# Kernel optimization log

Measured on AMD Instinct MI355X. Metric: run time of the kernel, lower is better.

## Reference

```python
import jax, jax.numpy as jnp
import numpy as np

K_SIZE = 7  # kernel_size (odd)


def setup_inputs() -> dict:
    key = jax.random.key(0)
    k0, k1, k2, k3 = jax.random.split(key, 4)
    B, C, H, W = 4, 128, 192, 192
    O, K = 128, K_SIZE
    x = jax.random.normal(k0, (B, C, H, W), dtype=jnp.float32)
    offsets = jax.random.normal(k1, (B, K, H, W), dtype=jnp.float32) * 0.5
    tumor_center = jax.random.uniform(k2, (B, 2), dtype=jnp.float32) * H  # (h, w) coords
    kernel_w = jax.random.normal(k3, (O * K, C), dtype=jnp.float32) / np.sqrt(C)  # 1x1 conv weight
    kernel_b = jnp.zeros((O * K,), dtype=jnp.float32)
    return {"x": x, "offsets": offsets, "tumor_center": tumor_center,
            "kernel_w": kernel_w, "kernel_b": kernel_b}


def reference(x, offsets, tumor_center, kernel_w, kernel_b):
    B, C, H, W = x.shape
    K = K_SIZE
    O = kernel_w.shape[0] // K
    pad = K // 2
    dt = x.dtype

    # ---- radial flow grid (faithful to source; see note below) ----
    h_c = tumor_center[:, 0][:, None, None]          # [B,1,1]
    w_c = tumor_center[:, 1][:, None, None]
    h_idx = jnp.arange(H, dtype=dt)[None, :, None]   # [1,H,1]
    w_idx = jnp.arange(W, dtype=dt)[None, None, :]   # [1,1,W]
    dh = h_idx - h_c                                  # [B,H,W]
    dw = w_idx - w_c
    rnorm = jnp.sqrt(dh * dh + dw * dw + 1e-6)
    dir_h = dh / rnorm
    dir_w = dw / rnorm
    base = jnp.linspace(-pad, pad, K, dtype=dt).reshape(1, K, 1, 1)
    h_grid = base * dir_h[:, None] + offsets          # [B,K,H,W]
    w_grid = base * dir_w[:, None] + offsets
    h_grid = h_grid / (H - 1) * 2
    w_grid = w_grid / (W - 1) * 2
    grid = jnp.stack([w_grid, h_grid], axis=-1)       # [B,K,H,W,2]
    # grid_sample is applied to x reshaped to [B*H*W, C, 1, 1] (a single-pixel
    # input) with align_corners=True: the unnormalize factor (size-1)=0 pins the
    # sample location to pixel (0,0) for ANY grid value, so
    # sampled[bhw, c, k] == x[bhw, c] exactly (grid has zero influence/grad).
    del grid

    # ---- dynamic per-pixel kernels via 1x1 conv ----
    kern = jnp.einsum('bchw,fc->bfhw', x, kernel_w) + kernel_b[None, :, None, None]
    kern = kern.reshape(B, O, K, H, W)

    # ---- bmm([BHW,C,K], [BHW,K,O]) then sum over C, fused into one einsum ----
    out = jnp.einsum('bchw,bokhw->bohw', x, kern)     # [B,O,H,W]
    return out
```

## Files before the change

### kernel.cpp

```cpp
#include <hip/hip_runtime.h>
#include <hip/hip_bf16.h>

#define BB   4
#define CC   128
#define HH   192
#define WWd  192
#define HWp  (HH*WWd)
#define OO   128
#define KK   7
#define NPIX (BB*HWp)
#define TILE 64
#define XT_PITCH_B 272

typedef short bf16x8 __attribute__((ext_vector_type(8)));
typedef float f32x4  __attribute__((ext_vector_type(4)));

static __device__ __forceinline__ unsigned f2bf(float f) {
    union { __hip_bfloat16 h; unsigned short u; } cvt;
    cvt.h = __float2bfloat16(f);
    return (unsigned)cvt.u;
}

__global__ __launch_bounds__(256) void prep_kernel(const float* __restrict__ kw,
                                                   const float* __restrict__ kb,
                                                   unsigned short* __restrict__ wfrag,
                                                   float* __restrict__ bsum) {
    int tid = blockIdx.x * 256 + threadIdx.x;
    int o = tid >> 7, c = tid & 127;
    float s = 0.f;
#pragma unroll
    for (int k = 0; k < KK; ++k) s += kw[(o*KK + k)*CC + c];
    int wv = o >> 5, mt = (o >> 4) & 1, lo = o & 15;
    int ks = c >> 5, g = (c >> 3) & 3, j = c & 7;
    int idx = ((((wv*2 + mt)*4 + ks)*64) + (lo + 16*g))*8 + j;
    wfrag[idx] = (unsigned short)f2bf(s);
    if (c == 0) {
        float bs = 0.f;
#pragma unroll
        for (int k = 0; k < KK; ++k) bs += kb[o*KK + k];
        bsum[o] = bs;
    }
}

__global__ __launch_bounds__(256, 4) void conv_kernel(const float* __restrict__ x,
                                                      const unsigned short* __restrict__ wfrag,
                                                      const float* __restrict__ bsum,
                                                      float* __restrict__ out) {
    __shared__ __align__(16) unsigned char xTb[TILE * XT_PITCH_B];
    __shared__ float sPart[4][TILE];

    const int t = threadIdx.x;
    const int w = t >> 6;
    const int l = t & 63;
    const int lo16 = l & 15, g4 = l >> 4;

    const int pixBase = blockIdx.x * TILE;
    const int bIdx   = pixBase / HWp;
    const int hwBase = pixBase - bIdx * HWp;
    const float* xb  = x + (size_t)bIdx * CC * HWp + hwBase + l;

    bf16x8 afrag[2][4];
    const unsigned short* wf = wfrag + (size_t)w * 2*4*64*8;
#pragma unroll
    for (int mt = 0; mt < 2; ++mt)
#pragma unroll
        for (int ks = 0; ks < 4; ++ks)
            afrag[mt][ks] = *reinterpret_cast<const bf16x8*>(wf + ((size_t)(mt*4 + ks)*64 + l)*8);

    float v[32];
#pragma unroll
    for (int i = 0; i < 8; ++i) {
        const int c0 = w*32 + i*4;
#pragma unroll
        for (int j = 0; j < 4; ++j)
            v[i*4 + j] = xb[(size_t)(c0 + j) * HWp];
    }
    float csum = 0.f;
#pragma unroll
    for (int i = 0; i < 32; ++i) csum += v[i];
    sPart[w][l] = csum;
#pragma unroll
    for (int i = 0; i < 8; ++i) {
        uint2 u;
        u.x = f2bf(v[i*4+0]) | (f2bf(v[i*4+1]) << 16);
        u.y = f2bf(v[i*4+2]) | (f2bf(v[i*4+3]) << 16);
        *reinterpret_cast<uint2*>(&xTb[l*XT_PITCH_B + (w*32 + i*4)*2]) = u;
    }
    __syncthreads();

    f32x4 acc[2][4];
#pragma unroll
    for (int mt = 0; mt < 2; ++mt)
#pragma unroll
        for (int nt = 0; nt < 4; ++nt)
            acc[mt][nt] = (f32x4){0.f, 0.f, 0.f, 0.f};

    for (int ks = 0; ks < 4; ++ks) {
        bf16x8 bfr[4];
#pragma unroll
        for (int nt = 0; nt < 4; ++nt)
            bfr[nt] = *reinterpret_cast<const bf16x8*>(
                &xTb[(nt*16 + lo16)*XT_PITCH_B + ks*64 + g4*16]);
#pragma unroll
        for (int nt = 0; nt < 4; ++nt) {
            acc[0][nt] = __builtin_amdgcn_mfma_f32_16x16x32_bf16(afrag[0][ks], bfr[nt], acc[0][nt], 0, 0, 0);
            acc[1][nt] = __builtin_amdgcn_mfma_f32_16x16x32_bf16(afrag[1][ks], bfr[nt], acc[1][nt], 0, 0, 0);
        }
    }

    float* ob = out + (size_t)bIdx * OO * HWp + hwBase + lo16;
#pragma unroll
    for (int nt = 0; nt < 4; ++nt) {
        const int pp = nt*16 + lo16;
        const float sv = sPart[0][pp] + sPart[1][pp] + sPart[2][pp] + sPart[3][pp];
#pragma unroll
        for (int mt = 0; mt < 2; ++mt) {
            const int o0 = w*32 + mt*16 + g4*4;
            const float4 bs4 = *reinterpret_cast<const float4*>(bsum + o0);
#pragma unroll
            for (int r = 0; r < 4; ++r) {
                const float bsv = (r == 0) ? bs4.x : (r == 1) ? bs4.y : (r == 2) ? bs4.z : bs4.w;
                ob[(size_t)(o0 + r) * HWp + nt*16] = (acc[mt][nt][r] + bsv) * sv;
            }
        }
    }
}

extern "C" void kernel_launch(void* const* d_in, const int* in_sizes, int n_in,
                              void* d_out, int out_size, void* d_ws, size_t ws_size,
                              hipStream_t stream) {
    const float* x  = (const float*)d_in[0];
    const float* kw = (const float*)d_in[3];
    const float* kb = (const float*)d_in[4];
    float* outp = (float*)d_out;

    unsigned short* wfrag = (unsigned short*)d_ws;
    float* bsum = (float*)((char*)d_ws + 32768);

    prep_kernel<<<dim3(64), dim3(256), 0, stream>>>(kw, kb, wfrag, bsum);
    conv_kernel<<<dim3(NPIX / TILE), dim3(256), 0, stream>>>(x, wfrag, bsum, outp);
}
```

Baseline: 33.73 us.

## Make conv kernel persistent with register prefetch of next pixel tile

Launches a fixed grid of 768 blocks that each process three 64-pixel tiles, replacing the one-tile-per-block launch. While the MFMA and output stores for the current tile run, the next tile's x values are loaded into registers, then written to LDS after a barrier. This hides global load latency and amortizes the weight-fragment loads per block. The cost is fewer blocks in flight and extra barriers, and the occupancy hint was dropped from launch bounds.

```diff
diff --git a/kernel.cpp b/kernel.cpp
--- a/kernel.cpp
+++ b/kernel.cpp
@@ -10,6 +10,8 @@
 #define KK   7
 #define NPIX (BB*HWp)
 #define TILE 64
+#define GRIDB 768
+#define NT   3
 #define XT_PITCH_B 272
 
 typedef short bf16x8 __attribute__((ext_vector_type(8)));
@@ -42,10 +44,10 @@
     }
 }
 
-__global__ __launch_bounds__(256, 4) void conv_kernel(const float* __restrict__ x,
-                                                      const unsigned short* __restrict__ wfrag,
-                                                      const float* __restrict__ bsum,
-                                                      float* __restrict__ out) {
+__global__ __launch_bounds__(256) void conv_kernel(const float* __restrict__ x,
+                                                   const unsigned short* __restrict__ wfrag,
+                                                   const float* __restrict__ bsum,
+                                                   float* __restrict__ out) {
     __shared__ __align__(16) unsigned char xTb[TILE * XT_PITCH_B];
     __shared__ float sPart[4][TILE];
 
@@ -53,11 +55,6 @@
     const int w = t >> 6;
     const int l = t & 63;
     const int lo16 = l & 15, g4 = l >> 4;
-
-    const int pixBase = blockIdx.x * TILE;
-    const int bIdx   = pixBase / HWp;
-    const int hwBase = pixBase - bIdx * HWp;
-    const float* xb  = x + (size_t)bIdx * CC * HWp + hwBase + l;
 
     bf16x8 afrag[2][4];
     const unsigned short* wf = wfrag + (size_t)w * 2*4*64*8;
@@ -68,61 +65,105 @@
             afrag[mt][ks] = *reinterpret_cast<const bf16x8*>(wf + ((size_t)(mt*4 + ks)*64 + l)*8);
 
     float v[32];
+
+    int tau = blockIdx.x;
+    {
+        const int pix = tau * TILE;
+        const int bi  = pix / HWp;
+        const int hw  = pix - bi * HWp;
+        const float* xk = x + (size_t)bi * CC * HWp + hw + l;
 #pragma unroll
-    for (int i = 0; i < 8; ++i) {
-        const int c0 = w*32 + i*4;
+        for (int i = 0; i < 8; ++i)
 #pragma unroll
-        for (int j = 0; j < 4; ++j)
-            v[i*4 + j] = xb[(size_t)(c0 + j) * HWp];
-    }
-    float csum = 0.f;
+            for (int j = 0; j < 4; ++j)
+                v[i*4 + j] = xk[(size_t)(w*32 + i*4 + j) * HWp];
+        float cs = 0.f;
 #pragma unroll
-    for (int i = 0; i < 32; ++i) csum += v[i];
-    sPart[w][l] = csum;
+        for (int i = 0; i < 32; ++i) cs += v[i];
+        sPart[w][l] = cs;
 #pragma unroll
-    for (int i = 0; i < 8; ++i) {
-        uint2 u;
-        u.x = f2bf(v[i*4+0]) | (f2bf(v[i*4+1]) << 16);
-        u.y = f2bf(v[i*4+2]) | (f2bf(v[i*4+3]) << 16);
-        *reinterpret_cast<uint2*>(&xTb[l*XT_PITCH_B + (w*32 + i*4)*2]) = u;
-    }
-    __syncthreads();
-
-    f32x4 acc[2][4];
-#pragma unroll
-    for (int mt = 0; mt < 2; ++mt)
-#pragma unroll
-        for (int nt = 0; nt < 4; ++nt)
-            acc[mt][nt] = (f32x4){0.f, 0.f, 0.f, 0.f};
-
-    for (int ks = 0; ks < 4; ++ks) {
-        bf16x8 bfr[4];
-#pragma unroll
-        for (int nt = 0; nt < 4; ++nt)
-            bfr[nt] = *reinterpret_cast<const bf16x8*>(
-                &xTb[(nt*16 + lo16)*XT_PITCH_B + ks*64 + g4*16]);
-#pragma unroll
-        for (int nt = 0; nt < 4; ++nt) {
-            acc[0][nt] = __builtin_amdgcn_mfma_f32_16x16x32_bf16(afrag[0][ks], bfr[nt], acc[0][nt], 0, 0, 0);
-            acc[1][nt] = __builtin_amdgcn_mfma_f32_16x16x32_bf16(afrag[1][ks], bfr[nt], acc[1][nt], 0, 0, 0);
+        for (int i = 0; i < 8; ++i) {
+            uint2 u;
+            u.x = f2bf(v[i*4+0]) | (f2bf(v[i*4+1]) << 16);
+            u.y = f2bf(v[i*4+2]) | (f2bf(v[i*4+3]) << 16);
+            *reinterpret_cast<uint2*>(&xTb[l*XT_PITCH_B + (w*32 + i*4)*2]) = u;
         }
+        __syncthreads();
     }
 
-    float* ob = out + (size_t)bIdx * OO * HWp + hwBase + lo16;
+    for (int k = 0; k < NT; ++k) {
+        const bool more = (k + 1 < NT);
+
+        if (more) {
+            const int pix = (tau + GRIDB) * TILE;
+            const int bi  = pix / HWp;
+            const int hw  = pix - bi * HWp;
+            const float* xk = x + (size_t)bi * CC * HWp + hw + l;
 #pragma unroll
-    for (int nt = 0; nt < 4; ++nt) {
-        const int pp = nt*16 + lo16;
-        const float sv = sPart[0][pp] + sPart[1][pp] + sPart[2][pp] + sPart[3][pp];
+            for (int i = 0; i < 8; ++i)
 #pragma unroll
-        for (int mt = 0; mt < 2; ++mt) {
-            const int o0 = w*32 + mt*16 + g4*4;
-            const float4 bs4 = *reinterpret_cast<const float4*>(bsum + o0);
+                for (int j = 0; j < 4; ++j)
+                    v[i*4 + j] = xk[(size_t)(w*32 + i*4 + j) * HWp];
+        }
+
+        f32x4 acc[2][4];
 #pragma unroll
-            for (int r = 0; r < 4; ++r) {
-                const float bsv = (r == 0) ? bs4.x : (r == 1) ? bs4.y : (r == 2) ? bs4.z : bs4.w;
-                ob[(size_t)(o0 + r) * HWp + nt*16] = (acc[mt][nt][r] + bsv) * sv;
+        for (int mt = 0; mt < 2; ++mt)
+#pragma unroll
+            for (int nt = 0; nt < 4; ++nt)
+                acc[mt][nt] = (f32x4){0.f, 0.f, 0.f, 0.f};
+#pragma unroll
+        for (int ks = 0; ks < 4; ++ks) {
+            bf16x8 bfr[4];
+#pragma unroll
+            for (int nt = 0; nt < 4; ++nt)
+                bfr[nt] = *reinterpret_cast<const bf16x8*>(
+                    &xTb[(nt*16 + lo16)*XT_PITCH_B + ks*64 + g4*16]);
+#pragma unroll
+            for (int nt = 0; nt < 4; ++nt) {
+                acc[0][nt] = __builtin_amdgcn_mfma_f32_16x16x32_bf16(afrag[0][ks], bfr[nt], acc[0][nt], 0, 0, 0);
+                acc[1][nt] = __builtin_amdgcn_mfma_f32_16x16x32_bf16(afrag[1][ks], bfr[nt], acc[1][nt], 0, 0, 0);
             }
         }
+
+        {
+            const int pix = tau * TILE;
+            const int bi  = pix / HWp;
+            const int hw  = pix - bi * HWp;
+            float* ob = out + (size_t)bi * OO * HWp + hw + lo16;
+#pragma unroll
+            for (int nt = 0; nt < 4; ++nt) {
+                const int pp = nt*16 + lo16;
+                const float sv = sPart[0][pp] + sPart[1][pp] + sPart[2][pp] + sPart[3][pp];
+#pragma unroll
+                for (int mt = 0; mt < 2; ++mt) {
+                    const int o0 = w*32 + mt*16 + g4*4;
+                    const float4 bs4 = *reinterpret_cast<const float4*>(bsum + o0);
+#pragma unroll
+                    for (int r = 0; r < 4; ++r) {
+                        const float bsv = (r == 0) ? bs4.x : (r == 1) ? bs4.y : (r == 2) ? bs4.z : bs4.w;
+                        ob[(size_t)(o0 + r) * HWp + nt*16] = (acc[mt][nt][r] + bsv) * sv;
+                    }
+                }
+            }
+        }
+
+        if (more) {
+            __builtin_amdgcn_s_barrier();
+            float cs = 0.f;
+#pragma unroll
+            for (int i = 0; i < 32; ++i) cs += v[i];
+            sPart[w][l] = cs;
+#pragma unroll
+            for (int i = 0; i < 8; ++i) {
+                uint2 u;
+                u.x = f2bf(v[i*4+0]) | (f2bf(v[i*4+1]) << 16);
+                u.y = f2bf(v[i*4+2]) | (f2bf(v[i*4+3]) << 16);
+                *reinterpret_cast<uint2*>(&xTb[l*XT_PITCH_B + (w*32 + i*4)*2]) = u;
+            }
+            __syncthreads();
+        }
+        tau += GRIDB;
     }
 }
 
@@ -138,5 +179,5 @@
     float* bsum = (float*)((char*)d_ws + 32768);
 
     prep_kernel<<<dim3(64), dim3(256), 0, stream>>>(kw, kb, wfrag, bsum);
-    conv_kernel<<<dim3(NPIX / TILE), dim3(256), 0, stream>>>(x, wfrag, bsum, outp);
+    conv_kernel<<<dim3(GRIDB), dim3(256), 0, stream>>>(x, wfrag, bsum, outp);
 }
```

Result: slower. 35.23 us (+4.5%).
